# Performance work log

Hardware: AMD Instinct MI355X
Metric: run time of the kernel (lower is better)

Reference implementation:

```python
import jax, jax.numpy as jnp
import numpy as np

D_MODEL = 128
NHEAD = 8
HEAD_DIM = D_MODEL // NHEAD  # 16
NUM_LAYERS = 7
NUM_LABELS = 2
N_NODES = 10000
N_EDGES = 160000
NEG_SLOPE = 0.2  # GATv2Conv default negative_slope


def setup_inputs() -> dict:
    key = jax.random.key(0)
    ks = jax.random.split(key, 10)
    s = 1.0 / np.sqrt(D_MODEL)
    inp = {}
    inp["x"] = jax.random.normal(ks[0], (N_NODES, D_MODEL), dtype=jnp.float32)
    inp["edge_index"] = jax.random.randint(ks[1], (2, N_EDGES), 0, N_NODES, dtype=jnp.int64)
    inp["nchunks"] = 8  # uniform extra chunk size -> chunk = NUM_LABELS + 8 = 10
    # per-layer GATv2 params, stacked on a leading layer axis
    inp["Wl"] = jax.random.normal(ks[2], (NUM_LAYERS, D_MODEL, NHEAD * HEAD_DIM), dtype=jnp.float32) * s
    inp["bl"] = jnp.zeros((NUM_LAYERS, NHEAD * HEAD_DIM), dtype=jnp.float32)
    inp["Wr"] = jax.random.normal(ks[3], (NUM_LAYERS, D_MODEL, NHEAD * HEAD_DIM), dtype=jnp.float32) * s
    inp["br"] = jnp.zeros((NUM_LAYERS, NHEAD * HEAD_DIM), dtype=jnp.float32)
    inp["att"] = jax.random.normal(ks[4], (NUM_LAYERS, NHEAD, HEAD_DIM), dtype=jnp.float32) * s
    inp["bias"] = jnp.zeros((NUM_LAYERS, NHEAD * HEAD_DIM), dtype=jnp.float32)
    # split head: Linear(d_model, 1)
    inp["w_head"] = jax.random.normal(ks[5], (D_MODEL, 1), dtype=jnp.float32) * s
    inp["b_head"] = jnp.zeros((1,), dtype=jnp.float32)
    return inp


def _gatv2_layer(x, src, dst, Wl, bl, Wr, br, att, bias):
    # GATv2: e_ij = a^T LeakyReLU(W_l x_j + W_r x_i); alpha = segment-softmax over dst; out_i = sum alpha * W_l x_j
    N = x.shape[0]
    xl = (x @ Wl + bl).reshape(N, NHEAD, HEAD_DIM)
    xr = (x @ Wr + br).reshape(N, NHEAD, HEAD_DIM)
    z = jax.nn.leaky_relu(xl[src] + xr[dst], NEG_SLOPE)          # [E, H, D]
    e = jnp.einsum('ehd,hd->eh', z, att)                          # [E, H]
    emax = jax.ops.segment_max(e, dst, num_segments=N)            # [N, H]
    ex = jnp.exp(e - emax[dst])
    denom = jax.ops.segment_sum(ex, dst, num_segments=N)          # [N, H]
    alpha = ex / (denom[dst] + 1e-16)                             # [E, H]
    out = jax.ops.segment_sum(alpha[..., None] * xl[src], dst, num_segments=N)  # [N, H, D]
    return out.reshape(N, NHEAD * HEAD_DIM) + bias


def reference(x, edge_index, nchunks, Wl, bl, Wr, br, att, bias, w_head, b_head):
    N = x.shape[0]
    loop = jnp.arange(N, dtype=edge_index.dtype)  # GATv2Conv add_self_loops=True
    src = jnp.concatenate([edge_index[0], loop])
    dst = jnp.concatenate([edge_index[1], loop])
    for i in range(NUM_LAYERS):
        x = _gatv2_layer(x, src, dst, Wl[i], bl[i], Wr[i], br[i], att[i], bias[i])
    # uniform split of size (NUM_LABELS + nchunks); keep first NUM_LABELS rows of each chunk
    chunk = NUM_LABELS + int(nchunks)
    xs = x.reshape(-1, chunk, D_MODEL)[:, :NUM_LABELS]            # [n_chunks, num_labels, d]
    out = (xs @ w_head + b_head)[..., 0]                          # [n_chunks, num_labels]
    return out
```

## Files before the change

### kernel.cpp

```cpp
#include <hip/hip_runtime.h>
#include <math.h>

#define NT 256

typedef __attribute__((ext_vector_type(8))) short bf16x8;
typedef __attribute__((ext_vector_type(4))) float f32x4;


__device__ inline int detect_is64(const int* __restrict__ ei) {
    int is64 = 1;
#pragma unroll
    for (int k = 1; k < 16; k += 2) is64 &= (ei[k] == 0);
    return is64;
}

__device__ inline void split1(float f, short& hi, short& lo) {
    unsigned u = __float_as_uint(f);
    hi = (short)(u >> 16);
    float fl = f - __uint_as_float(u & 0xffff0000u);
    lo = (short)(__float_as_uint(fl) >> 16);
}

__device__ inline void cvt8(const float4& a, const float4& b, bf16x8& hi, bf16x8& lo) {
    float f[8] = {a.x, a.y, a.z, a.w, b.x, b.y, b.z, b.w};
#pragma unroll
    for (int j = 0; j < 8; j++) {
        unsigned u = __float_as_uint(f[j]);
        hi[j] = (short)(u >> 16);
        float fl = f[j] - __uint_as_float(u & 0xffff0000u);
        lo[j] = (short)(__float_as_uint(fl) >> 16);
    }
}


__global__ __launch_bounds__(256) void count_prep(const int* __restrict__ ei, int E, int N,
                                                  int* __restrict__ deg,
                                                  const float* __restrict__ Wl,
                                                  const float* __restrict__ Wr,
                                                  short* __restrict__ Whi,
                                                  short* __restrict__ Wlo) {
    __shared__ float Wt[128][17];
    int t = threadIdx.x;
    if (blockIdx.x < 112) {
        int l = blockIdx.x >> 4;
        int tile = blockIdx.x & 15;
        int c0 = tile * 16;
        const float* Wsrc = (c0 < 128) ? Wl + (size_t)l * 16384 : Wr + (size_t)l * 16384;
        int cbase = (c0 < 128) ? c0 : c0 - 128;
#pragma unroll
        for (int it = 0; it < 8; it++) {
            int idx = it * 256 + t;
            int k = idx >> 4, c = idx & 15;
            Wt[k][c] = Wsrc[(size_t)k * 128 + cbase + c];
        }
        __syncthreads();
        int kt = t >> 6, lane = t & 63, q = (lane >> 4), cl = lane & 15;
        bf16x8 hi, lo;
#pragma unroll
        for (int j = 0; j < 8; j++) {
            short h, lw;
            split1(Wt[kt * 32 + q * 8 + j][cl], h, lw);
            hi[j] = h; lo[j] = lw;
        }
        size_t off = ((((size_t)l * 16 + tile) * 4 + kt) * 64 + lane) * 8;
        *(bf16x8*)(Whi + off) = hi;
        *(bf16x8*)(Wlo + off) = lo;
    } else {
        int e = (blockIdx.x - 112) * 256 + t;
        if (e >= E) return;
        int is64 = detect_is64(ei);
        long long pos = (long long)E + e;
        int d = ei[is64 ? 2 * pos : pos];
        if ((unsigned)d < (unsigned)N) atomicAdd(&deg[d], 1);
    }
}

__global__ __launch_bounds__(256) void scan_kernel(const int* __restrict__ deg,
                                                   int* __restrict__ off,
                                                   int* __restrict__ cur, int N) {
    __shared__ int wsum[4];
    int t = threadIdx.x;
    int per = (N + 255) >> 8;
    int b0 = t * per;
    int s = 0;
    for (int k = 0; k < per; k++) {
        int idx = b0 + k;
        if (idx < N) s += deg[idx];
    }
    int lane = t & 63, w = t >> 6;
    int v = s;
#pragma unroll
    for (int o = 1; o < 64; o <<= 1) {
        int u = __shfl_up(v, o, 64);
        if (lane >= o) v += u;
    }
    if (lane == 63) wsum[w] = v;
    __syncthreads();
    if (t == 0) {
        int r = 0;
#pragma unroll
        for (int j = 0; j < 4; j++) { int xx = wsum[j]; wsum[j] = r; r += xx; }
        off[N] = r;
    }
    __syncthreads();
    int run = v - s + wsum[w];
    for (int k = 0; k < per; k++) {
        int idx = b0 + k;
        if (idx < N) {
            off[idx] = run;
            cur[idx] = run;
            run += deg[idx];
        }
    }
}

__global__ void fill_kernel(const int* __restrict__ ei, int E, int N,
                            int* __restrict__ cur, int* __restrict__ esrc) {
    int e = blockIdx.x * blockDim.x + threadIdx.x;
    if (e >= E) return;
    int is64 = detect_is64(ei);
    long long spos = e, dpos = (long long)E + e;
    int s = ei[is64 ? 2 * spos : spos];
    int d = ei[is64 ? 2 * dpos : dpos];
    if ((unsigned)d >= (unsigned)N || (unsigned)s >= (unsigned)N) return;
    int p = atomicAdd(&cur[d], 1);
    esrc[p] = s;
}


__global__ __launch_bounds__(512)
__attribute__((amdgpu_waves_per_eu(2, 2)))
void gemm_xlxr(const float* __restrict__ x,
               const short* __restrict__ WhiL,
               const short* __restrict__ WloL,
               const float* __restrict__ blv,
               const float* __restrict__ brv,
               float* __restrict__ xl,
               float* __restrict__ xr,
               int N, int ntiles) {
    int t = threadIdx.x;
    int w = t >> 6, lane = t & 63, q = lane >> 4, cl = lane & 15;

    bf16x8 Bh[2][4], Bl[2][4];
    float biasv[2];
    float* outp[2];
    int colc[2];
#pragma unroll
    for (int nt = 0; nt < 2; nt++) {
        int tile = w * 2 + nt;
        int col = tile * 16 + cl;
        if (col < 128) { biasv[nt] = blv[col]; outp[nt] = xl; colc[nt] = col; }
        else           { biasv[nt] = brv[col - 128]; outp[nt] = xr; colc[nt] = col - 128; }
#pragma unroll
        for (int kt = 0; kt < 4; kt++) {
            size_t off = (((size_t)tile * 4 + kt) * 64 + lane) * 8;
            Bh[nt][kt] = *(const bf16x8*)(WhiL + off);
            Bl[nt][kt] = *(const bf16x8*)(WloL + off);
        }
    }

    int rt = blockIdx.x;
    if (rt >= ntiles) return;
    float4 cur[8], nxt[8];
    {
        int row = rt * 16 + cl;
        if (row >= N) row = N - 1;
        const float* ap = x + (size_t)row * 128 + q * 8;
#pragma unroll
        for (int kt = 0; kt < 4; kt++) {
            cur[2 * kt]     = *(const float4*)(ap + kt * 32);
            cur[2 * kt + 1] = *(const float4*)(ap + kt * 32 + 4);
        }
    }

    for (; rt < ntiles; rt += gridDim.x) {
        int rn = rt + gridDim.x;
        if (rn < ntiles) {
            int row = rn * 16 + cl;
            if (row >= N) row = N - 1;
            const float* ap = x + (size_t)row * 128 + q * 8;
#pragma unroll
            for (int kt = 0; kt < 4; kt++) {
                nxt[2 * kt]     = *(const float4*)(ap + kt * 32);
                nxt[2 * kt + 1] = *(const float4*)(ap + kt * 32 + 4);
            }
        }

        bf16x8 Ah[4], Al[4];
#pragma unroll
        for (int kt = 0; kt < 4; kt++) cvt8(cur[2 * kt], cur[2 * kt + 1], Ah[kt], Al[kt]);

        f32x4 acc0 = {0.f, 0.f, 0.f, 0.f}, acc1 = {0.f, 0.f, 0.f, 0.f};
#pragma unroll
        for (int kt = 0; kt < 4; kt++) {
            acc0 = __builtin_amdgcn_mfma_f32_16x16x32_bf16(Ah[kt], Bh[0][kt], acc0, 0, 0, 0);
            acc1 = __builtin_amdgcn_mfma_f32_16x16x32_bf16(Ah[kt], Bh[1][kt], acc1, 0, 0, 0);
            acc0 = __builtin_amdgcn_mfma_f32_16x16x32_bf16(Al[kt], Bh[0][kt], acc0, 0, 0, 0);
            acc1 = __builtin_amdgcn_mfma_f32_16x16x32_bf16(Al[kt], Bh[1][kt], acc1, 0, 0, 0);
            acc0 = __builtin_amdgcn_mfma_f32_16x16x32_bf16(Ah[kt], Bl[0][kt], acc0, 0, 0, 0);
            acc1 = __builtin_amdgcn_mfma_f32_16x16x32_bf16(Ah[kt], Bl[1][kt], acc1, 0, 0, 0);
        }

#pragma unroll
        for (int nt = 0; nt < 2; nt++) {
            f32x4 a = nt ? acc1 : acc0;
#pragma unroll
            for (int r = 0; r < 4; r++) {
                int row = rt * 16 + q * 4 + r;
                if (row < N) outp[nt][(size_t)row * 128 + colc[nt]] = a[r] + biasv[nt];
            }
        }
#pragma unroll
        for (int j = 0; j < 8; j++) cur[j] = nxt[j];
    }
}


__global__ __launch_bounds__(256) void gat_agg(const float4* __restrict__ xl4,
                                               const float4* __restrict__ xr4,
                                               const int* __restrict__ off,
                                               const int* __restrict__ esrc,
                                               const float4* __restrict__ att4,
                                               const float4* __restrict__ bias4,
                                               float4* __restrict__ out4, int N) {
    int lane = threadIdx.x & 63;
    int sub = lane >> 4;
    int cl = lane & 15;
    int i = blockIdx.x * 4 + (threadIdx.x >> 6);
    if (i >= N) return;

    float4 xrA = xr4[(size_t)i * 32 + 2 * cl];
    float4 xrB = xr4[(size_t)i * 32 + 2 * cl + 1];
    float4 atA = att4[2 * cl];
    float4 atB = att4[2 * cl + 1];
    int start = off[i];
    int total = off[i + 1] - start + 1;
    int groups = (total + 3) >> 2;

    int k0 = sub;
    int s0 = (k0 < total) ? ((k0 == 0) ? i : esrc[start + k0 - 1]) : i;
    int k1 = 4 + sub;
    int s1 = (k1 < total) ? esrc[start + k1 - 1] : i;
    float4 v0A = xl4[(size_t)s0 * 32 + 2 * cl];
    float4 v0B = xl4[(size_t)s0 * 32 + 2 * cl + 1];
    int k2 = 8 + sub;
    int s2 = (k2 < total) ? esrc[start + k2 - 1] : i;
    float4 v1A = xl4[(size_t)s1 * 32 + 2 * cl];
    float4 v1B = xl4[(size_t)s1 * 32 + 2 * cl + 1];

    float s = 0.f;
    float4 aA = make_float4(0.f, 0.f, 0.f, 0.f);
    float4 aB = make_float4(0.f, 0.f, 0.f, 0.f);

    for (int g = 0; g < groups; g++) {
        int k3 = 4 * (g + 3) + sub;
        int s3 = (k3 < total) ? esrc[start + k3 - 1] : i;
        float4 v2A = xl4[(size_t)s2 * 32 + 2 * cl];
        float4 v2B = xl4[(size_t)s2 * 32 + 2 * cl + 1];

        int kc = 4 * g + sub;
        int valid = kc < total;
        float z0 = v0A.x + xrA.x, z1 = v0A.y + xrA.y, z2 = v0A.z + xrA.z, z3 = v0A.w + xrA.w;
        float z4 = v0B.x + xrB.x, z5 = v0B.y + xrB.y, z6 = v0B.z + xrB.z, z7 = v0B.w + xrB.w;
        z0 = (z0 > 0.f) ? z0 : 0.2f * z0;
        z1 = (z1 > 0.f) ? z1 : 0.2f * z1;
        z2 = (z2 > 0.f) ? z2 : 0.2f * z2;
        z3 = (z3 > 0.f) ? z3 : 0.2f * z3;
        z4 = (z4 > 0.f) ? z4 : 0.2f * z4;
        z5 = (z5 > 0.f) ? z5 : 0.2f * z5;
        z6 = (z6 > 0.f) ? z6 : 0.2f * z6;
        z7 = (z7 > 0.f) ? z7 : 0.2f * z7;
        float p = z0 * atA.x + z1 * atA.y + z2 * atA.z + z3 * atA.w
                + z4 * atB.x + z5 * atB.y + z6 * atB.z + z7 * atB.w;
        p += __shfl_xor(p, 1, 64);
        p = fminf(fmaxf(p, -80.f), 80.f);
        float wgt = valid ? __expf(p) : 0.f;
        s += wgt;
        aA.x += wgt * v0A.x; aA.y += wgt * v0A.y; aA.z += wgt * v0A.z; aA.w += wgt * v0A.w;
        aB.x += wgt * v0B.x; aB.y += wgt * v0B.y; aB.z += wgt * v0B.z; aB.w += wgt * v0B.w;

        v0A = v1A; v0B = v1B;
        v1A = v2A; v1B = v2B;
        s2 = s3;
    }

#pragma unroll
    for (int o = 16; o <= 32; o <<= 1) {
        s += __shfl_xor(s, o, 64);
        aA.x += __shfl_xor(aA.x, o, 64); aA.y += __shfl_xor(aA.y, o, 64);
        aA.z += __shfl_xor(aA.z, o, 64); aA.w += __shfl_xor(aA.w, o, 64);
        aB.x += __shfl_xor(aB.x, o, 64); aB.y += __shfl_xor(aB.y, o, 64);
        aB.z += __shfl_xor(aB.z, o, 64); aB.w += __shfl_xor(aB.w, o, 64);
    }
    if (sub == 0) {
        float inv = 1.f / (s + 1e-16f);
        float4 bA = bias4[2 * cl], bB = bias4[2 * cl + 1];
        float4 oA, oB;
        oA.x = aA.x * inv + bA.x; oA.y = aA.y * inv + bA.y;
        oA.z = aA.z * inv + bA.z; oA.w = aA.w * inv + bA.w;
        oB.x = aB.x * inv + bB.x; oB.y = aB.y * inv + bB.y;
        oB.z = aB.z * inv + bB.z; oB.w = aB.w * inv + bB.w;
        out4[(size_t)i * 32 + 2 * cl] = oA;
        out4[(size_t)i * 32 + 2 * cl + 1] = oB;
    }
}


__global__ __launch_bounds__(128) void head_kernel(const float* __restrict__ x,
                                                   const float* __restrict__ w,
                                                   const float* __restrict__ bh,
                                                   const int* __restrict__ nch,
                                                   float* __restrict__ out) {
    __shared__ float r[2];
    int b = blockIdx.x, t = threadIdx.x;
    int chunk = 2 + nch[0];
    int row = (b >> 1) * chunk + (b & 1);
    float p = x[(size_t)row * 128 + t] * w[t];
#pragma unroll
    for (int o = 32; o >= 1; o >>= 1) p += __shfl_xor(p, o, 64);
    if ((t & 63) == 0) r[t >> 6] = p;
    __syncthreads();
    if (t == 0) out[b] = r[0] + r[1] + bh[0];
}


extern "C" void kernel_launch(void* const* d_in, const int* in_sizes, int n_in,
                              void* d_out, int out_size, void* d_ws, size_t ws_size,
                              hipStream_t stream) {
    const float* x0 = (const float*)d_in[0];
    const int* ei = (const int*)d_in[1];
    const int* nchunks = (const int*)d_in[2];
    const float* Wl = (const float*)d_in[3];
    const float* bl = (const float*)d_in[4];
    const float* Wr = (const float*)d_in[5];
    const float* br = (const float*)d_in[6];
    const float* att = (const float*)d_in[7];
    const float* bias = (const float*)d_in[8];
    const float* wh = (const float*)d_in[9];
    const float* bh = (const float*)d_in[10];

    const int D = 128;
    int N = in_sizes[0] / D;
    int E = in_sizes[1] / 2;
    int ntiles = (N + 15) / 16;

    size_t fN = (size_t)N * D;
    const size_t WFRAG = 16 * 4 * 64 * 8;
    float* xl = (float*)d_ws;
    float* xr = xl + fN;
    float* xA = xr + fN;
    float* xB = xA + fN;
    short* Whi = (short*)(xB + fN);
    short* Wlo = Whi + 7 * WFRAG;
    int* deg = (int*)(Wlo + 7 * WFRAG);
    int* off = deg + N;
    int* cur = off + N + 1;
    int* esrc = cur + N;

    hipMemsetAsync(deg, 0, (size_t)N * sizeof(int), stream);
    count_prep<<<112 + (E + NT - 1) / NT, NT, 0, stream>>>(ei, E, N, deg, Wl, Wr, Whi, Wlo);
    scan_kernel<<<1, 256, 0, stream>>>(deg, off, cur, N);
    fill_kernel<<<(E + NT - 1) / NT, NT, 0, stream>>>(ei, E, N, cur, esrc);

    int aggblocks = (N + 3) / 4;
    const float* xc = x0;
    float* xn = xA;
    for (int l = 0; l < 7; l++) {
        gemm_xlxr<<<256, 512, 0, stream>>>(xc, Whi + (size_t)l * WFRAG, Wlo + (size_t)l * WFRAG,
                                           bl + (size_t)l * D, br + (size_t)l * D,
                                           xl, xr, N, ntiles);
        gat_agg<<<aggblocks, 256, 0, stream>>>((const float4*)xl, (const float4*)xr, off, esrc,
                                               (const float4*)(att + (size_t)l * D),
                                               (const float4*)(bias + (size_t)l * D),
                                               (float4*)xn, N);
        xc = xn;
        xn = (xn == xA) ? xB : xA;
    }
    head_kernel<<<out_size, 128, 0, stream>>>(xc, wh, bh, nchunks, (float*)d_out);
}
```

Baseline: 319.3 us.

## Fuse all GAT layers and head into one persistent kernel with grid barriers

Result: slower. 879.7 us (+175.5%).

```diff
diff --git a/kernel.cpp b/kernel.cpp
--- a/kernel.cpp
+++ b/kernel.cpp
@@ -30,6 +30,54 @@
         float fl = f[j] - __uint_as_float(u & 0xffff0000u);
         lo[j] = (short)(__float_as_uint(fl) >> 16);
     }
+}
+
+__device__ inline void prep_w_block(int bid, const float* __restrict__ Wl,
+                                    const float* __restrict__ Wr,
+                                    short* __restrict__ Whi, short* __restrict__ Wlo,
+                                    float (*Wt)[17], int t) {
+    int l = bid >> 4;
+    int tile = bid & 15;
+    int c0 = tile * 16;
+    const float* Wsrc = (c0 < 128) ? Wl + (size_t)l * 16384 : Wr + (size_t)l * 16384;
+    int cbase = (c0 < 128) ? c0 : c0 - 128;
+#pragma unroll
+    for (int it = 0; it < 8; it++) {
+        int idx = it * 256 + t;
+        int k = idx >> 4, c = idx & 15;
+        Wt[k][c] = Wsrc[(size_t)k * 128 + cbase + c];
+    }
+    __syncthreads();
+    int kt = t >> 6, lane = t & 63, q = (lane >> 4), cl = lane & 15;
+    bf16x8 hi, lo;
+#pragma unroll
+    for (int j = 0; j < 8; j++) {
+        short h, lw;
+        split1(Wt[kt * 32 + q * 8 + j][cl], h, lw);
+        hi[j] = h; lo[j] = lw;
+    }
+    size_t off = ((((size_t)l * 16 + tile) * 4 + kt) * 64 + lane) * 8;
+    *(bf16x8*)(Whi + off) = hi;
+    *(bf16x8*)(Wlo + off) = lo;
+}
+
+
+__device__ inline void gbar(int* cnt, int* gen, int nblk) {
+    __syncthreads();
+    if (threadIdx.x == 0) {
+        __threadfence();
+        int g = __hip_atomic_load(gen, __ATOMIC_ACQUIRE, __HIP_MEMORY_SCOPE_AGENT);
+        int prev = __hip_atomic_fetch_add(cnt, 1, __ATOMIC_ACQ_REL, __HIP_MEMORY_SCOPE_AGENT);
+        if (prev == nblk - 1) {
+            __hip_atomic_store(cnt, 0, __ATOMIC_RELAXED, __HIP_MEMORY_SCOPE_AGENT);
+            __hip_atomic_fetch_add(gen, 1, __ATOMIC_RELEASE, __HIP_MEMORY_SCOPE_AGENT);
+        } else {
+            while (__hip_atomic_load(gen, __ATOMIC_ACQUIRE, __HIP_MEMORY_SCOPE_AGENT) == g)
+                __builtin_amdgcn_s_sleep(8);
+        }
+        __threadfence();
+    }
+    __syncthreads();
 }
 
 
@@ -42,29 +90,7 @@
     __shared__ float Wt[128][17];
     int t = threadIdx.x;
     if (blockIdx.x < 112) {
-        int l = blockIdx.x >> 4;
-        int tile = blockIdx.x & 15;
-        int c0 = tile * 16;
-        const float* Wsrc = (c0 < 128) ? Wl + (size_t)l * 16384 : Wr + (size_t)l * 16384;
-        int cbase = (c0 < 128) ? c0 : c0 - 128;
-#pragma unroll
-        for (int it = 0; it < 8; it++) {
-            int idx = it * 256 + t;
-            int k = idx >> 4, c = idx & 15;
-            Wt[k][c] = Wsrc[(size_t)k * 128 + cbase + c];
-        }
-        __syncthreads();
-        int kt = t >> 6, lane = t & 63, q = (lane >> 4), cl = lane & 15;
-        bf16x8 hi, lo;
-#pragma unroll
-        for (int j = 0; j < 8; j++) {
-            short h, lw;
-            split1(Wt[kt * 32 + q * 8 + j][cl], h, lw);
-            hi[j] = h; lo[j] = lw;
-        }
-        size_t off = ((((size_t)l * 16 + tile) * 4 + kt) * 64 + lane) * 8;
-        *(bf16x8*)(Whi + off) = hi;
-        *(bf16x8*)(Wlo + off) = lo;
+        prep_w_block(blockIdx.x, Wl, Wr, Whi, Wlo, Wt, t);
     } else {
         int e = (blockIdx.x - 112) * 256 + t;
         if (e >= E) return;
@@ -115,7 +141,9 @@
 }
 
 __global__ void fill_kernel(const int* __restrict__ ei, int E, int N,
-                            int* __restrict__ cur, int* __restrict__ esrc) {
+                            int* __restrict__ cur, int* __restrict__ esrc,
+                            int* __restrict__ bar) {
+    if (blockIdx.x == 0 && threadIdx.x == 0) { bar[0] = 0; bar[1] = 0; }
     int e = blockIdx.x * blockDim.x + threadIdx.x;
     if (e >= E) return;
     int is64 = detect_is64(ei);
@@ -128,199 +156,217 @@
 }
 
 
-__global__ __launch_bounds__(512)
-__attribute__((amdgpu_waves_per_eu(2, 2)))
-void gemm_xlxr(const float* __restrict__ x,
-               const short* __restrict__ WhiL,
-               const short* __restrict__ WloL,
-               const float* __restrict__ blv,
-               const float* __restrict__ brv,
-               float* __restrict__ xl,
-               float* __restrict__ xr,
-               int N, int ntiles) {
+__global__ __launch_bounds__(512) void layers_mega(
+    const float* __restrict__ x0,
+    const short* __restrict__ Whi, const short* __restrict__ Wlo,
+    const float* __restrict__ bl, const float* __restrict__ br,
+    const float* __restrict__ att, const float* __restrict__ bias,
+    const float* __restrict__ wh, const float* __restrict__ bh,
+    const int* __restrict__ nch,
+    const int* __restrict__ off, const int* __restrict__ esrc,
+    float* __restrict__ xl, float* __restrict__ xr,
+    float* __restrict__ xA, float* __restrict__ xB,
+    float* __restrict__ head_out,
+    int N, int ntiles, int* __restrict__ bar) {
+
     int t = threadIdx.x;
-    int w = t >> 6, lane = t & 63, q = lane >> 4, cl = lane & 15;
-
-    bf16x8 Bh[2][4], Bl[2][4];
-    float biasv[2];
-    float* outp[2];
-    int colc[2];
-#pragma unroll
-    for (int nt = 0; nt < 2; nt++) {
-        int tile = w * 2 + nt;
-        int col = tile * 16 + cl;
-        if (col < 128) { biasv[nt] = blv[col]; outp[nt] = xl; colc[nt] = col; }
-        else           { biasv[nt] = brv[col - 128]; outp[nt] = xr; colc[nt] = col - 128; }
-#pragma unroll
-        for (int kt = 0; kt < 4; kt++) {
-            size_t off = (((size_t)tile * 4 + kt) * 64 + lane) * 8;
-            Bh[nt][kt] = *(const bf16x8*)(WhiL + off);
-            Bl[nt][kt] = *(const bf16x8*)(WloL + off);
-        }
-    }
-
-    int rt = blockIdx.x;
-    if (rt >= ntiles) return;
-    float4 cur[8], nxt[8];
-    {
-        int row = rt * 16 + cl;
-        if (row >= N) row = N - 1;
-        const float* ap = x + (size_t)row * 128 + q * 8;
-#pragma unroll
-        for (int kt = 0; kt < 4; kt++) {
-            cur[2 * kt]     = *(const float4*)(ap + kt * 32);
-            cur[2 * kt + 1] = *(const float4*)(ap + kt * 32 + 4);
-        }
-    }
-
-    for (; rt < ntiles; rt += gridDim.x) {
-        int rn = rt + gridDim.x;
-        if (rn < ntiles) {
-            int row = rn * 16 + cl;
-            if (row >= N) row = N - 1;
-            const float* ap = x + (size_t)row * 128 + q * 8;
-#pragma unroll
-            for (int kt = 0; kt < 4; kt++) {
-                nxt[2 * kt]     = *(const float4*)(ap + kt * 32);
-                nxt[2 * kt + 1] = *(const float4*)(ap + kt * 32 + 4);
+    int b = blockIdx.x;
+    int wave = t >> 6, lane = t & 63;
+    int q = lane >> 4, cl = lane & 15;
+    int gw = b * 8 + wave;
+    const int GW = gridDim.x * 8;
+    const int NB = gridDim.x;
+
+    const float* xc = x0;
+    float* xn = xA;
+
+    for (int l = 0; l < 7; l++) {
+        {
+            const short* WhiL = Whi + (size_t)l * 32768;
+            const short* WloL = Wlo + (size_t)l * 32768;
+            const float* blv = bl + (size_t)l * 128;
+            const float* brv = br + (size_t)l * 128;
+
+            bf16x8 Bh[2][4], Bl_[2][4];
+            float biasv[2];
+            float* outp[2];
+            int colc[2];
+#pragma unroll
+            for (int nt = 0; nt < 2; nt++) {
+                int tile = wave * 2 + nt;
+                int col = tile * 16 + cl;
+                if (col < 128) { biasv[nt] = blv[col]; outp[nt] = xl; colc[nt] = col; }
+                else           { biasv[nt] = brv[col - 128]; outp[nt] = xr; colc[nt] = col - 128; }
+#pragma unroll
+                for (int kt = 0; kt < 4; kt++) {
+                    size_t woff = (((size_t)tile * 4 + kt) * 64 + lane) * 8;
+                    Bh[nt][kt] = *(const bf16x8*)(WhiL + woff);
+                    Bl_[nt][kt] = *(const bf16x8*)(WloL + woff);
+                }
+            }
+
+            int rt = b;
+            float4 cur[8], nxt[8];
+            if (rt < ntiles) {
+                int row = rt * 16 + cl;
+                if (row >= N) row = N - 1;
+                const float* ap = xc + (size_t)row * 128 + q * 8;
+#pragma unroll
+                for (int kt = 0; kt < 4; kt++) {
+                    cur[2 * kt]     = *(const float4*)(ap + kt * 32);
+                    cur[2 * kt + 1] = *(const float4*)(ap + kt * 32 + 4);
+                }
+            }
+            for (; rt < ntiles; rt += NB) {
+                int rn = rt + NB;
+                if (rn < ntiles) {
+                    int row = rn * 16 + cl;
+                    if (row >= N) row = N - 1;
+                    const float* ap = xc + (size_t)row * 128 + q * 8;
+#pragma unroll
+                    for (int kt = 0; kt < 4; kt++) {
+                        nxt[2 * kt]     = *(const float4*)(ap + kt * 32);
+                        nxt[2 * kt + 1] = *(const float4*)(ap + kt * 32 + 4);
+                    }
+                }
+                bf16x8 Ah[4], Al[4];
+#pragma unroll
+                for (int kt = 0; kt < 4; kt++) cvt8(cur[2 * kt], cur[2 * kt + 1], Ah[kt], Al[kt]);
+                f32x4 acc0 = {0.f, 0.f, 0.f, 0.f}, acc1 = {0.f, 0.f, 0.f, 0.f};
+#pragma unroll
+                for (int kt = 0; kt < 4; kt++) {
+                    acc0 = __builtin_amdgcn_mfma_f32_16x16x32_bf16(Ah[kt], Bh[0][kt], acc0, 0, 0, 0);
+                    acc1 = __builtin_amdgcn_mfma_f32_16x16x32_bf16(Ah[kt], Bh[1][kt], acc1, 0, 0, 0);
+                    acc0 = __builtin_amdgcn_mfma_f32_16x16x32_bf16(Al[kt], Bh[0][kt], acc0, 0, 0, 0);
+                    acc1 = __builtin_amdgcn_mfma_f32_16x16x32_bf16(Al[kt], Bh[1][kt], acc1, 0, 0, 0);
+                    acc0 = __builtin_amdgcn_mfma_f32_16x16x32_bf16(Ah[kt], Bl_[0][kt], acc0, 0, 0, 0);
+                    acc1 = __builtin_amdgcn_mfma_f32_16x16x32_bf16(Ah[kt], Bl_[1][kt], acc1, 0, 0, 0);
+                }
+#pragma unroll
+                for (int nt = 0; nt < 2; nt++) {
+                    f32x4 a = nt ? acc1 : acc0;
+#pragma unroll
+                    for (int r = 0; r < 4; r++) {
+                        int orow = rt * 16 + q * 4 + r;
+                        if (orow < N) outp[nt][(size_t)orow * 128 + colc[nt]] = a[r] + biasv[nt];
+                    }
+                }
+#pragma unroll
+                for (int j = 0; j < 8; j++) cur[j] = nxt[j];
             }
         }
-
-        bf16x8 Ah[4], Al[4];
-#pragma unroll
-        for (int kt = 0; kt < 4; kt++) cvt8(cur[2 * kt], cur[2 * kt + 1], Ah[kt], Al[kt]);
-
-        f32x4 acc0 = {0.f, 0.f, 0.f, 0.f}, acc1 = {0.f, 0.f, 0.f, 0.f};
-#pragma unroll
-        for (int kt = 0; kt < 4; kt++) {
-            acc0 = __builtin_amdgcn_mfma_f32_16x16x32_bf16(Ah[kt], Bh[0][kt], acc0, 0, 0, 0);
-            acc1 = __builtin_amdgcn_mfma_f32_16x16x32_bf16(Ah[kt], Bh[1][kt], acc1, 0, 0, 0);
-            acc0 = __builtin_amdgcn_mfma_f32_16x16x32_bf16(Al[kt], Bh[0][kt], acc0, 0, 0, 0);
-            acc1 = __builtin_amdgcn_mfma_f32_16x16x32_bf16(Al[kt], Bh[1][kt], acc1, 0, 0, 0);
-            acc0 = __builtin_amdgcn_mfma_f32_16x16x32_bf16(Ah[kt], Bl[0][kt], acc0, 0, 0, 0);
-            acc1 = __builtin_amdgcn_mfma_f32_16x16x32_bf16(Ah[kt], Bl[1][kt], acc1, 0, 0, 0);
-        }
-
-#pragma unroll
-        for (int nt = 0; nt < 2; nt++) {
-            f32x4 a = nt ? acc1 : acc0;
-#pragma unroll
-            for (int r = 0; r < 4; r++) {
-                int row = rt * 16 + q * 4 + r;
-                if (row < N) outp[nt][(size_t)row * 128 + colc[nt]] = a[r] + biasv[nt];
+        gbar(&bar[0], &bar[1], NB);
+
+        {
+            const float4* xl4 = (const float4*)xl;
+            const float4* xr4 = (const float4*)xr;
+            const float4* att4 = (const float4*)(att + (size_t)l * 128);
+            const float4* bias4 = (const float4*)(bias + (size_t)l * 128);
+            float4* out4 = (float4*)xn;
+            int sub = lane >> 4;
+            int do_head = (l == 6);
+
+            for (int i = gw; i < N; i += GW) {
+                float4 xrA = xr4[(size_t)i * 32 + 2 * cl];
+                float4 xrB = xr4[(size_t)i * 32 + 2 * cl + 1];
+                float4 atA = att4[2 * cl];
+                float4 atB = att4[2 * cl + 1];
+                int start = off[i];
+                int total = off[i + 1] - start + 1;
+                int groups = (total + 3) >> 2;
+
+                int k0 = sub;
+                int s0 = (k0 < total) ? ((k0 == 0) ? i : esrc[start + k0 - 1]) : i;
+                int k1 = 4 + sub;
+                int s1 = (k1 < total) ? esrc[start + k1 - 1] : i;
+                float4 v0A = xl4[(size_t)s0 * 32 + 2 * cl];
+                float4 v0B = xl4[(size_t)s0 * 32 + 2 * cl + 1];
+                int k2 = 8 + sub;
+                int s2 = (k2 < total) ? esrc[start + k2 - 1] : i;
+                float4 v1A = xl4[(size_t)s1 * 32 + 2 * cl];
+                float4 v1B = xl4[(size_t)s1 * 32 + 2 * cl + 1];
+
+                float s = 0.f;
+                float4 aA = make_float4(0.f, 0.f, 0.f, 0.f);
+                float4 aB = make_float4(0.f, 0.f, 0.f, 0.f);
+
+                for (int g = 0; g < groups; g++) {
+                    int k3 = 4 * (g + 3) + sub;
+                    int s3 = (k3 < total) ? esrc[start + k3 - 1] : i;
+                    float4 v2A = xl4[(size_t)s2 * 32 + 2 * cl];
+                    float4 v2B = xl4[(size_t)s2 * 32 + 2 * cl + 1];
+
+                    int kc = 4 * g + sub;
+                    int valid = kc < total;
+                    float z0 = v0A.x + xrA.x, z1 = v0A.y + xrA.y, z2 = v0A.z + xrA.z, z3 = v0A.w + xrA.w;
+                    float z4 = v0B.x + xrB.x, z5 = v0B.y + xrB.y, z6 = v0B.z + xrB.z, z7 = v0B.w + xrB.w;
+                    z0 = (z0 > 0.f) ? z0 : 0.2f * z0;
+                    z1 = (z1 > 0.f) ? z1 : 0.2f * z1;
+                    z2 = (z2 > 0.f) ? z2 : 0.2f * z2;
+                    z3 = (z3 > 0.f) ? z3 : 0.2f * z3;
+                    z4 = (z4 > 0.f) ? z4 : 0.2f * z4;
+                    z5 = (z5 > 0.f) ? z5 : 0.2f * z5;
+                    z6 = (z6 > 0.f) ? z6 : 0.2f * z6;
+                    z7 = (z7 > 0.f) ? z7 : 0.2f * z7;
+                    float p = z0 * atA.x + z1 * atA.y + z2 * atA.z + z3 * atA.w
+                            + z4 * atB.x + z5 * atB.y + z6 * atB.z + z7 * atB.w;
+                    p += __shfl_xor(p, 1, 64);
+                    p = fminf(fmaxf(p, -80.f), 80.f);
+                    float wgt = valid ? __expf(p) : 0.f;
+                    s += wgt;
+                    aA.x += wgt * v0A.x; aA.y += wgt * v0A.y; aA.z += wgt * v0A.z; aA.w += wgt * v0A.w;
+                    aB.x += wgt * v0B.x; aB.y += wgt * v0B.y; aB.z += wgt * v0B.z; aB.w += wgt * v0B.w;
+
+                    v0A = v1A; v0B = v1B;
+                    v1A = v2A; v1B = v2B;
+                    s2 = s3;
+                }
+
+#pragma unroll
+                for (int o = 16; o <= 32; o <<= 1) {
+                    s += __shfl_xor(s, o, 64);
+                    aA.x += __shfl_xor(aA.x, o, 64); aA.y += __shfl_xor(aA.y, o, 64);
+                    aA.z += __shfl_xor(aA.z, o, 64); aA.w += __shfl_xor(aA.w, o, 64);
+                    aB.x += __shfl_xor(aB.x, o, 64); aB.y += __shfl_xor(aB.y, o, 64);
+                    aB.z += __shfl_xor(aB.z, o, 64); aB.w += __shfl_xor(aB.w, o, 64);
+                }
+
+                float inv = 1.f / (s + 1e-16f);
+                float4 bA = bias4[2 * cl], bB = bias4[2 * cl + 1];
+                float4 oA, oB;
+                oA.x = aA.x * inv + bA.x; oA.y = aA.y * inv + bA.y;
+                oA.z = aA.z * inv + bA.z; oA.w = aA.w * inv + bA.w;
+                oB.x = aB.x * inv + bB.x; oB.y = aB.y * inv + bB.y;
+                oB.z = aB.z * inv + bB.z; oB.w = aB.w * inv + bB.w;
+
+                if (!do_head) {
+                    if (sub == 0) {
+                        out4[(size_t)i * 32 + 2 * cl] = oA;
+                        out4[(size_t)i * 32 + 2 * cl + 1] = oB;
+                    }
+                } else {
+                    int chunk = 2 + nch[0];
+                    int ci = i / chunk;
+                    int m = i - ci * chunk;
+                    if (m < 2) {
+                        const float4* wv = (const float4*)wh;
+                        float4 wA = wv[2 * cl], wB = wv[2 * cl + 1];
+                        float p = oA.x * wA.x + oA.y * wA.y + oA.z * wA.z + oA.w * wA.w
+                                + oB.x * wB.x + oB.y * wB.y + oB.z * wB.z + oB.w * wB.w;
+                        p += __shfl_xor(p, 1, 64);
+                        p += __shfl_xor(p, 2, 64);
+                        p += __shfl_xor(p, 4, 64);
+                        p += __shfl_xor(p, 8, 64);
+                        if (lane == 0) head_out[ci * 2 + m] = p + bh[0];
+                    }
+                }
             }
         }
-#pragma unroll
-        for (int j = 0; j < 8; j++) cur[j] = nxt[j];
-    }
-}
-
-
-__global__ __launch_bounds__(256) void gat_agg(const float4* __restrict__ xl4,
-                                               const float4* __restrict__ xr4,
-                                               const int* __restrict__ off,
-                                               const int* __restrict__ esrc,
-                                               const float4* __restrict__ att4,
-                                               const float4* __restrict__ bias4,
-                                               float4* __restrict__ out4, int N) {
-    int lane = threadIdx.x & 63;
-    int sub = lane >> 4;
-    int cl = lane & 15;
-    int i = blockIdx.x * 4 + (threadIdx.x >> 6);
-    if (i >= N) return;
-
-    float4 xrA = xr4[(size_t)i * 32 + 2 * cl];
-    float4 xrB = xr4[(size_t)i * 32 + 2 * cl + 1];
-    float4 atA = att4[2 * cl];
-    float4 atB = att4[2 * cl + 1];
-    int start = off[i];
-    int total = off[i + 1] - start + 1;
-    int groups = (total + 3) >> 2;
-
-    int k0 = sub;
-    int s0 = (k0 < total) ? ((k0 == 0) ? i : esrc[start + k0 - 1]) : i;
-    int k1 = 4 + sub;
-    int s1 = (k1 < total) ? esrc[start + k1 - 1] : i;
-    float4 v0A = xl4[(size_t)s0 * 32 + 2 * cl];
-    float4 v0B = xl4[(size_t)s0 * 32 + 2 * cl + 1];
-    int k2 = 8 + sub;
-    int s2 = (k2 < total) ? esrc[start + k2 - 1] : i;
-    float4 v1A = xl4[(size_t)s1 * 32 + 2 * cl];
-    float4 v1B = xl4[(size_t)s1 * 32 + 2 * cl + 1];
-
-    float s = 0.f;
-    float4 aA = make_float4(0.f, 0.f, 0.f, 0.f);
-    float4 aB = make_float4(0.f, 0.f, 0.f, 0.f);
-
-    for (int g = 0; g < groups; g++) {
-        int k3 = 4 * (g + 3) + sub;
-        int s3 = (k3 < total) ? esrc[start + k3 - 1] : i;
-        float4 v2A = xl4[(size_t)s2 * 32 + 2 * cl];
-        float4 v2B = xl4[(size_t)s2 * 32 + 2 * cl + 1];
-
-        int kc = 4 * g + sub;
-        int valid = kc < total;
-        float z0 = v0A.x + xrA.x, z1 = v0A.y + xrA.y, z2 = v0A.z + xrA.z, z3 = v0A.w + xrA.w;
-        float z4 = v0B.x + xrB.x, z5 = v0B.y + xrB.y, z6 = v0B.z + xrB.z, z7 = v0B.w + xrB.w;
-        z0 = (z0 > 0.f) ? z0 : 0.2f * z0;
-        z1 = (z1 > 0.f) ? z1 : 0.2f * z1;
-        z2 = (z2 > 0.f) ? z2 : 0.2f * z2;
-        z3 = (z3 > 0.f) ? z3 : 0.2f * z3;
-        z4 = (z4 > 0.f) ? z4 : 0.2f * z4;
-        z5 = (z5 > 0.f) ? z5 : 0.2f * z5;
-        z6 = (z6 > 0.f) ? z6 : 0.2f * z6;
-        z7 = (z7 > 0.f) ? z7 : 0.2f * z7;
-        float p = z0 * atA.x + z1 * atA.y + z2 * atA.z + z3 * atA.w
-                + z4 * atB.x + z5 * atB.y + z6 * atB.z + z7 * atB.w;
-        p += __shfl_xor(p, 1, 64);
-        p = fminf(fmaxf(p, -80.f), 80.f);
-        float wgt = valid ? __expf(p) : 0.f;
-        s += wgt;
-        aA.x += wgt * v0A.x; aA.y += wgt * v0A.y; aA.z += wgt * v0A.z; aA.w += wgt * v0A.w;
-        aB.x += wgt * v0B.x; aB.y += wgt * v0B.y; aB.z += wgt * v0B.z; aB.w += wgt * v0B.w;
-
-        v0A = v1A; v0B = v1B;
-        v1A = v2A; v1B = v2B;
-        s2 = s3;
-    }
-
-#pragma unroll
-    for (int o = 16; o <= 32; o <<= 1) {
-        s += __shfl_xor(s, o, 64);
-        aA.x += __shfl_xor(aA.x, o, 64); aA.y += __shfl_xor(aA.y, o, 64);
-        aA.z += __shfl_xor(aA.z, o, 64); aA.w += __shfl_xor(aA.w, o, 64);
-        aB.x += __shfl_xor(aB.x, o, 64); aB.y += __shfl_xor(aB.y, o, 64);
-        aB.z += __shfl_xor(aB.z, o, 64); aB.w += __shfl_xor(aB.w, o, 64);
-    }
-    if (sub == 0) {
-        float inv = 1.f / (s + 1e-16f);
-        float4 bA = bias4[2 * cl], bB = bias4[2 * cl + 1];
-        float4 oA, oB;
-        oA.x = aA.x * inv + bA.x; oA.y = aA.y * inv + bA.y;
-        oA.z = aA.z * inv + bA.z; oA.w = aA.w * inv + bA.w;
-        oB.x = aB.x * inv + bB.x; oB.y = aB.y * inv + bB.y;
-        oB.z = aB.z * inv + bB.z; oB.w = aB.w * inv + bB.w;
-        out4[(size_t)i * 32 + 2 * cl] = oA;
-        out4[(size_t)i * 32 + 2 * cl + 1] = oB;
-    }
-}
-
-
-__global__ __launch_bounds__(128) void head_kernel(const float* __restrict__ x,
-                                                   const float* __restrict__ w,
-                                                   const float* __restrict__ bh,
-                                                   const int* __restrict__ nch,
-                                                   float* __restrict__ out) {
-    __shared__ float r[2];
-    int b = blockIdx.x, t = threadIdx.x;
-    int chunk = 2 + nch[0];
-    int row = (b >> 1) * chunk + (b & 1);
-    float p = x[(size_t)row * 128 + t] * w[t];
-#pragma unroll
-    for (int o = 32; o >= 1; o >>= 1) p += __shfl_xor(p, o, 64);
-    if ((t & 63) == 0) r[t >> 6] = p;
-    __syncthreads();
-    if (t == 0) out[b] = r[0] + r[1] + bh[0];
+        if (l < 6) gbar(&bar[0], &bar[1], NB);
+
+        xc = xn;
+        xn = (xn == xA) ? xB : xA;
+    }
 }
 
 
@@ -356,25 +402,14 @@
     int* off = deg + N;
     int* cur = off + N + 1;
     int* esrc = cur + N;
+    int* bar = esrc + E;
 
     hipMemsetAsync(deg, 0, (size_t)N * sizeof(int), stream);
     count_prep<<<112 + (E + NT - 1) / NT, NT, 0, stream>>>(ei, E, N, deg, Wl, Wr, Whi, Wlo);
     scan_kernel<<<1, 256, 0, stream>>>(deg, off, cur, N);
-    fill_kernel<<<(E + NT - 1) / NT, NT, 0, stream>>>(ei, E, N, cur, esrc);
-
-    int aggblocks = (N + 3) / 4;
-    const float* xc = x0;
-    float* xn = xA;
-    for (int l = 0; l < 7; l++) {
-        gemm_xlxr<<<256, 512, 0, stream>>>(xc, Whi + (size_t)l * WFRAG, Wlo + (size_t)l * WFRAG,
-                                           bl + (size_t)l * D, br + (size_t)l * D,
-                                           xl, xr, N, ntiles);
-        gat_agg<<<aggblocks, 256, 0, stream>>>((const float4*)xl, (const float4*)xr, off, esrc,
-                                               (const float4*)(att + (size_t)l * D),
-                                               (const float4*)(bias + (size_t)l * D),
-                                               (float4*)xn, N);
-        xc = xn;
-        xn = (xn == xA) ? xB : xA;
-    }
-    head_kernel<<<out_size, 128, 0, stream>>>(xc, wh, bh, nchunks, (float*)d_out);
-}
+    fill_kernel<<<(E + NT - 1) / NT, NT, 0, stream>>>(ei, E, N, cur, esrc, bar);
+
+    layers_mega<<<256, 512, 0, stream>>>(x0, Whi, Wlo, bl, br, att, bias, wh, bh, nchunks,
+                                         off, esrc, xl, xr, xA, xB,
+                                         (float*)d_out, N, ntiles, bar);
+}
```
